# Kernel tuning notes

Hardware: AMD Instinct MI355X
Metric: run time of the kernel (lower is better)

## Reference

```python
import jax, jax.numpy as jnp
import numpy as np

B, S, DM = 2, 2048, 2048
H, KVH, HD = 16, 4, 128
REP = H // KVH  # kv_repeat_factor = 4
ROPE_BASE = 10000.0
EPS = 1e-6


def setup_inputs() -> dict:
    key = jax.random.key(0)
    k0, k1, k2, k3, k4 = jax.random.split(key, 5)
    w = lambda k, o, i: jax.random.normal(k, (o, i), jnp.float32) * (1.0 / np.sqrt(i))
    return {
        "x": jax.random.normal(k0, (B, S, DM), jnp.float32),
        "Wq": w(k1, H * HD, DM),
        "Wk": w(k2, KVH * HD, DM),
        "Wv": w(k3, KVH * HD, DM),
        "Wo": w(k4, DM, H * HD),
    }


def _rope_tables(seq_len, dim):
    inv_freq = 1.0 / (ROPE_BASE ** (jnp.arange(0, dim, 2, dtype=jnp.float32) / dim))
    t = jnp.arange(seq_len, dtype=jnp.float32)
    freqs = jnp.outer(t, inv_freq)            # [S, dim/2]
    emb = jnp.concatenate([freqs, freqs], -1)  # [S, dim]
    return jnp.cos(emb), jnp.sin(emb)


def _rotate_half(x):
    d = x.shape[-1] // 2
    return jnp.concatenate([-x[..., d:], x[..., :d]], axis=-1)


def reference(x, Wq, Wk, Wv, Wo):
    bsz, seq_len, _ = x.shape
    # projections (torch Linear: y = x @ W.T)
    q = (x @ Wq.T).reshape(bsz, seq_len, H, HD).transpose(0, 2, 1, 3)    # [B,H,S,D]
    k = (x @ Wk.T).reshape(bsz, seq_len, KVH, HD).transpose(0, 2, 1, 3)  # [B,KVH,S,D]
    v = (x @ Wv.T).reshape(bsz, seq_len, KVH, HD).transpose(0, 2, 1, 3)
    # rotary embeddings
    cos, sin = _rope_tables(seq_len, HD)  # [S,D]
    cos, sin = cos[None, None], sin[None, None]
    q = q * cos + _rotate_half(q) * sin
    k = k * cos + _rotate_half(k) * sin
    # GQA repeat (repeat_interleave on head dim)
    k = jnp.repeat(k, REP, axis=1)  # [B,H,S,D]
    v = jnp.repeat(v, REP, axis=1)
    # feature map
    qf = jax.nn.elu(q) + 1.0
    kf = jax.nn.elu(k) + 1.0
    # causal linear attention: recurrent kv-state scan over time
    qf_t = qf.transpose(2, 0, 1, 3)  # [S,B,H,D]
    kf_t = kf.transpose(2, 0, 1, 3)
    v_t = v.transpose(2, 0, 1, 3)

    def step(carry, inp):
        state, z = carry                       # [B,H,D,D], [B,H,D]
        q_s, k_s, v_s = inp                    # each [B,H,D]
        state = state + k_s[..., :, None] * v_s[..., None, :]
        z = z + k_s
        num = jnp.einsum('bhe,bhed->bhd', q_s, state)
        den = jnp.einsum('bhe,bhe->bh', q_s, z)[..., None] + EPS
        return (state, z), num / den

    init = (jnp.zeros((bsz, H, HD, HD), x.dtype), jnp.zeros((bsz, H, HD), x.dtype))
    _, out = jax.lax.scan(step, init, (qf_t, kf_t, v_t))  # [S,B,H,D]
    out = out.transpose(1, 0, 2, 3).reshape(bsz, seq_len, H * HD)
    return out @ Wo.T
```

## Files before the change

### kernel.cpp

```cpp
#include <hip/hip_runtime.h>
#include <math.h>
#include <stdint.h>

#define B_ 2
#define S_ 2048
#define H_ 16
#define KVH_ 4
#define HD_ 128
#define NC_ 16
#define CHK_ 128
#define EPS_ 1e-6f
#define GK_ 2048
#define NT_ (GK_ / 32)

typedef __attribute__((ext_vector_type(8))) short short8;
typedef __attribute__((ext_vector_type(4))) float f32x4;

#define GLOAD16(gsrc, sdst) \
    __builtin_amdgcn_global_load_lds((const __attribute__((address_space(1))) unsigned int*)(gsrc), \
                                     (__attribute__((address_space(3))) unsigned int*)(sdst), 16, 0, 0)

static __device__ __forceinline__ float bf2f(unsigned int u) {
    return __uint_as_float(u << 16);
}

static __device__ __forceinline__ void pack8(const float* v, uint4& hi, uint4& lo) {
    unsigned int h[4], l[4];
#pragma unroll
    for (int w = 0; w < 4; w++) {
        unsigned int b0 = __float_as_uint(v[2 * w]);
        unsigned int b1 = __float_as_uint(v[2 * w + 1]);
        unsigned int h0 = b0 & 0xFFFF0000u, h1 = b1 & 0xFFFF0000u;
        h[w] = (h0 >> 16) | h1;
        float r0 = v[2 * w] - __uint_as_float(h0);
        float r1 = v[2 * w + 1] - __uint_as_float(h1);
        l[w] = (__float_as_uint(r0) >> 16) | (__float_as_uint(r1) & 0xFFFF0000u);
    }
    hi = make_uint4(h[0], h[1], h[2], h[3]);
    lo = make_uint4(l[0], l[1], l[2], l[3]);
}

static __device__ __forceinline__ void split8_frag(const float* p, short8& hi, short8& lo) {
#pragma unroll
    for (int e = 0; e < 8; e++) {
        unsigned int b = __float_as_uint(p[e]);
        unsigned int h = b & 0xFFFF0000u;
        hi[e] = (short)(h >> 16);
        float r = p[e] - __uint_as_float(h);
        lo[e] = (short)(__float_as_uint(r) >> 16);
    }
}

__global__ __launch_bounds__(256) void rope_tables_k(float* __restrict__ cost,
                                                     float* __restrict__ sint) {
    int idx = blockIdx.x * 256 + threadIdx.x;
    int j = idx & 63;
    int s = idx >> 6;
    float inv_freq = powf(10000.0f, -(float)(2 * j) / 128.0f);
    float f = (float)s * inv_freq;
    cost[idx] = cosf(f);
    sint[idx] = sinf(f);
}

__global__ __launch_bounds__(256) void split_k(const float* __restrict__ in,
                                               unsigned int* __restrict__ outp, int ngrp)
{
    int g = blockIdx.x * 256 + threadIdx.x;
    if (g >= ngrp) return;
    const float* p = in + (size_t)g * 8;
    float x[8];
    *(float4*)&x[0] = *(const float4*)p;
    *(float4*)&x[4] = *(const float4*)(p + 4);
    uint4 hi, lo;
    pack8(x, hi, lo);
    unsigned int* op = outp + (size_t)g * 8;
    *(uint4*)op       = hi;
    *(uint4*)(op + 4) = lo;
}

__global__ __launch_bounds__(256, 2) void gemm3_k(
    const char* __restrict__ Apk, const char* __restrict__ W0,
    const char* __restrict__ W1, const char* __restrict__ W2,
    float* __restrict__ Y, int ldY, int nend0, int nend1, int nbx)
{
    __shared__ __attribute__((aligned(16))) char smem[65536];

    int nwg = gridDim.x;
    int bid = blockIdx.x;
    int swz = (bid & 7) * (nwg >> 3) + (bid >> 3);
    int by = swz / nbx, bx = swz % nbx;
    const int m0 = by * 128, n0 = bx * 128;

    const char* Wsel;
    int nw;
    if (n0 < nend0)      { Wsel = W0; nw = n0; }
    else if (n0 < nend1) { Wsel = W1; nw = n0 - nend0; }
    else                 { Wsel = W2; nw = n0 - nend1; }

    const int tid = threadIdx.x;
    const int lane = tid & 63;
    const int wv = tid >> 6;
    const int wr = wv >> 1, wc = wv & 1;

    const int r8 = lane >> 3, sl = lane & 7;
    const char* ap[4];
    const char* wp[4];
    int adst[4], wdst[4];
#pragma unroll
    for (int i = 0; i < 4; i++) {
        int rowA = wv * 32 + i * 8 + r8;
        ap[i] = Apk + (size_t)(m0 + rowA) * (GK_ * 4) + (size_t)((sl ^ (rowA & 7)) * 16);
        wp[i] = Wsel + (size_t)(nw + rowA) * (GK_ * 4) + (size_t)((sl ^ (rowA & 7)) * 16);
        adst[i] = wv * 4096 + i * 1024;
        wdst[i] = 16384 + wv * 4096 + i * 1024;
    }

    const int lrow = lane & 15, lg = lane >> 4, lc7 = lane & 7;
    const int aoff = (wr * 64 + lrow) * 128 + ((((lg << 1)) ^ lc7) << 4);
    const int woff = 16384 + (wc * 64 + lrow) * 128 + ((((lg << 1)) ^ lc7) << 4);

    f32x4 acc[4][4];
#pragma unroll
    for (int i = 0; i < 4; i++)
#pragma unroll
        for (int j = 0; j < 4; j++) acc[i][j] = (f32x4)(0.f);

#pragma unroll
    for (int i = 0; i < 4; i++) {
        GLOAD16(ap[i], smem + adst[i]);
        GLOAD16(wp[i], smem + wdst[i]);
    }
    __syncthreads();

    for (int kt = 0; kt < NT_; ++kt) {
        const int cur = kt & 1;
        if (kt + 1 < NT_) {
            const size_t koff = (size_t)(kt + 1) * 128;
            const int nb = (cur ^ 1) * 32768;
#pragma unroll
            for (int i = 0; i < 4; i++) {
                GLOAD16(ap[i] + koff, smem + nb + adst[i]);
                GLOAD16(wp[i] + koff, smem + nb + wdst[i]);
            }
        }
        const char* sb = smem + cur * 32768;
        short8 ah[4], al[4], bh[4], bl[4];
#pragma unroll
        for (int f = 0; f < 4; f++) {
            ah[f] = *(const short8*)(sb + (aoff)        + f * 2048);
            al[f] = *(const short8*)(sb + (aoff ^ 16)   + f * 2048);
            bh[f] = *(const short8*)(sb + (woff)        + f * 2048);
            bl[f] = *(const short8*)(sb + (woff ^ 16)   + f * 2048);
        }
#pragma unroll
        for (int i = 0; i < 4; i++)
#pragma unroll
            for (int j = 0; j < 4; j++) {
                acc[i][j] = __builtin_amdgcn_mfma_f32_16x16x32_bf16(ah[i], bh[j], acc[i][j], 0, 0, 0);
                acc[i][j] = __builtin_amdgcn_mfma_f32_16x16x32_bf16(ah[i], bl[j], acc[i][j], 0, 0, 0);
                acc[i][j] = __builtin_amdgcn_mfma_f32_16x16x32_bf16(al[i], bh[j], acc[i][j], 0, 0, 0);
            }
        __syncthreads();
    }

#pragma unroll
    for (int i = 0; i < 4; i++) {
        int r0 = m0 + wr * 64 + i * 16 + lg * 4;
#pragma unroll
        for (int j = 0; j < 4; j++) {
            int cc = n0 + wc * 64 + j * 16 + lrow;
            f32x4 v = acc[i][j];
            Y[(size_t)(r0 + 0) * ldY + cc] = v[0];
            Y[(size_t)(r0 + 1) * ldY + cc] = v[1];
            Y[(size_t)(r0 + 2) * ldY + cc] = v[2];
            Y[(size_t)(r0 + 3) * ldY + cc] = v[3];
        }
    }
}

__global__ __launch_bounds__(256) void rope_feat_k(
    const float* __restrict__ qkv, const float* __restrict__ cost,
    const float* __restrict__ sint, char* __restrict__ qfpk, char* __restrict__ kfpk)
{
    int idx = blockIdx.x * 256 + threadIdx.x;
    int g = idx & 15;
    int t = idx >> 4;
    int hh = t % 20;
    int t2 = t / 20;
    int s = t2 % S_;
    int b = t2 / S_;
    const float* row = qkv + (size_t)(b * S_ + s) * 3072;
    int col;
    char* outp;
    if (hh < H_) {
        col = hh * HD_;
        outp = qfpk + ((size_t)(b * H_ + hh) * S_ + s) * 512;
    } else {
        int kv = hh - H_;
        col = 2048 + kv * HD_;
        outp = kfpk + ((size_t)(b * KVH_ + kv) * S_ + s) * 512;
    }
    int d0 = g * 8;
    int dp = (g < 8) ? d0 + 64 : d0 - 64;
    int j0 = (g < 8) ? d0 : d0 - 64;
    float xa[8], xb[8], o[8];
    *(float4*)&xa[0] = *(const float4*)(row + col + d0);
    *(float4*)&xa[4] = *(const float4*)(row + col + d0 + 4);
    *(float4*)&xb[0] = *(const float4*)(row + col + dp);
    *(float4*)&xb[4] = *(const float4*)(row + col + dp + 4);
#pragma unroll
    for (int e = 0; e < 8; e++) {
        float cs = cost[s * 64 + j0 + e];
        float sn = sint[s * 64 + j0 + e];
        float v = (g < 8) ? (xa[e] * cs - xb[e] * sn) : (xa[e] * cs + xb[e] * sn);
        o[e] = v > 0.f ? v + 1.f : expf(v);
    }
    uint4 hi, lo;
    pack8(o, hi, lo);
    *(uint4*)(outp + g * 32)      = hi;
    *(uint4*)(outp + g * 32 + 16) = lo;
}

__global__ __launch_bounds__(256) void copy_v_k(const float* __restrict__ qkv,
                                                float* __restrict__ vv,
                                                char* __restrict__ vtpk)
{
    __shared__ __attribute__((aligned(16))) float Vt[CHK_][HD_ + 4];
    int bx = blockIdx.x;
    int st = bx & 15;
    int bkv = bx >> 4;
    int b = bkv >> 2, kv = bkv & 3;
    int tid = threadIdx.x;
#pragma unroll
    for (int it = 0; it < 16; it++) {
        int idx = it * 256 + tid;
        int r = idx >> 5, c4 = idx & 31;
        float4 v = *(const float4*)(qkv + (size_t)(b * S_ + st * CHK_ + r) * 3072 + 2560 + kv * HD_ + c4 * 4);
        *(float4*)(vv + ((size_t)bkv * S_ + st * CHK_ + r) * HD_ + c4 * 4) = v;
        *(float4*)&Vt[r][c4 * 4] = v;
    }
    __syncthreads();
#pragma unroll
    for (int it = 0; it < 2; it++) {
        int t2 = it * 256 + tid;
        int d = t2 & 127, sg = t2 >> 7;
#pragma unroll
        for (int kk = 0; kk < 4; kk++) {
            int kgl = sg * 4 + kk;
            float f[8];
#pragma unroll
            for (int e = 0; e < 8; e++) f[e] = Vt[kgl * 8 + e][d];
            uint4 hi, lo;
            pack8(f, hi, lo);
            char* op = vtpk + (size_t)bkv * 1048576 + (size_t)d * 8192 + (size_t)(st * 16 + kgl) * 32;
            *(uint4*)op        = hi;
            *(uint4*)(op + 16) = lo;
        }
    }
}

__global__ __launch_bounds__(256) void chunk_kv_k(
    const char* __restrict__ kfpk, const float* __restrict__ vv,
    float* __restrict__ kvc, float* __restrict__ zc)
{
    int bx = blockIdx.x;
    int c = bx % NC_;
    int bkv = bx / NC_;
    const char* kp = kfpk + ((size_t)bkv * S_ + c * CHK_) * 512;
    const float* vp = vv + ((size_t)bkv * S_ + c * CHK_) * HD_;
    __shared__ __attribute__((aligned(16))) float ks[CHK_][HD_ + 4];
    __shared__ __attribute__((aligned(16))) float vs[CHK_][HD_ + 4];
    int tid = threadIdx.x, tx = tid & 15, ty = tid >> 4;
#pragma unroll
    for (int it = 0; it < 8; it++) {
        int idx = it * 256 + tid;
        int r = idx >> 4, kg = idx & 15;
        const uint4* sp = (const uint4*)(kp + (size_t)r * 512 + kg * 32);
        uint4 hi = sp[0], lo = sp[1];
        float* d = &ks[r][kg * 8];
        d[0] = bf2f(hi.x & 0xFFFFu) + bf2f(lo.x & 0xFFFFu);
        d[1] = bf2f(hi.x >> 16)     + bf2f(lo.x >> 16);
        d[2] = bf2f(hi.y & 0xFFFFu) + bf2f(lo.y & 0xFFFFu);
        d[3] = bf2f(hi.y >> 16)     + bf2f(lo.y >> 16);
        d[4] = bf2f(hi.z & 0xFFFFu) + bf2f(lo.z & 0xFFFFu);
        d[5] = bf2f(hi.z >> 16)     + bf2f(lo.z >> 16);
        d[6] = bf2f(hi.w & 0xFFFFu) + bf2f(lo.w & 0xFFFFu);
        d[7] = bf2f(hi.w >> 16)     + bf2f(lo.w >> 16);
    }
#pragma unroll
    for (int it = 0; it < 16; it++) {
        int idx = it * 256 + tid;
        int r = idx >> 5, c4 = idx & 31;
        *(float4*)&vs[r][c4 * 4] = *(const float4*)(vp + (size_t)r * HD_ + c4 * 4);
    }
    __syncthreads();
    float acc[8][8];
#pragma unroll
    for (int i = 0; i < 8; i++)
#pragma unroll
        for (int j = 0; j < 8; j++) acc[i][j] = 0.f;
    for (int j = 0; j < CHK_; j++) {
        float a[8], b[8];
        *(float4*)&a[0] = *(const float4*)&ks[j][ty * 8];
        *(float4*)&a[4] = *(const float4*)&ks[j][ty * 8 + 4];
        *(float4*)&b[0] = *(const float4*)&vs[j][tx * 8];
        *(float4*)&b[4] = *(const float4*)&vs[j][tx * 8 + 4];
#pragma unroll
        for (int i = 0; i < 8; i++)
#pragma unroll
            for (int jj = 0; jj < 8; jj++)
                acc[i][jj] = fmaf(a[i], b[jj], acc[i][jj]);
    }
    float* outp = kvc + (size_t)bx * (HD_ * HD_);
#pragma unroll
    for (int i = 0; i < 8; i++) {
        float* op = outp + (size_t)(ty * 8 + i) * HD_ + tx * 8;
        *(float4*)op       = make_float4(acc[i][0], acc[i][1], acc[i][2], acc[i][3]);
        *(float4*)(op + 4) = make_float4(acc[i][4], acc[i][5], acc[i][6], acc[i][7]);
    }
    if (tid < CHK_) {
        float z = 0.f;
        for (int j = 0; j < CHK_; j++) z += ks[j][tid];
        zc[(size_t)bx * HD_ + tid] = z;
    }
}

__global__ __launch_bounds__(256) void chunk_scan_k(const float* __restrict__ kvc,
                                                    char* __restrict__ kvct,
                                                    float* __restrict__ zc)
{
    int bx = blockIdx.x;
    int bkv = bx >> 3, dg = bx & 7;
    int tid = threadIdx.x;
    int d = dg * 16 + (tid & 15);
    int g8 = tid >> 4;
    float acc[8];
#pragma unroll
    for (int i = 0; i < 8; i++) acc[i] = 0.f;
    float zacc = 0.f;
    for (int c = 0; c < NC_; c++) {
        size_t cb = (size_t)(bkv * NC_ + c);
        const float* p = kvc + cb * 16384;
        float cur[8];
#pragma unroll
        for (int i = 0; i < 8; i++) cur[i] = p[(g8 * 8 + i) * 128 + d];
        uint4 hi, lo;
        pack8(acc, hi, lo);
        char* op = kvct + cb * 65536 + (size_t)d * 512 + g8 * 32;
        *(uint4*)op        = hi;
        *(uint4*)(op + 16) = lo;
#pragma unroll
        for (int i = 0; i < 8; i++) acc[i] += cur[i];
        if (tid < 16) {
            float* zp = zc + cb * 128 + dg * 16 + tid;
            float zcur = *zp;
            *zp = zacc;
            zacc += zcur;
        }
    }
}

__global__ __launch_bounds__(256, 1) void chunk_out_k(
    const char* __restrict__ qfpk, const char* __restrict__ kfpk,
    const char* __restrict__ vtpk, const char* __restrict__ kvct,
    const float* __restrict__ zc, char* __restrict__ attnpk)
{
    __shared__ __attribute__((aligned(16))) char smem[100864];
    char*  stA  = smem;
    char*  stB  = smem + 16384;
    float* Pf   = (float*)(smem + 32768);
    float* zs   = (float*)(smem + 98304);
    float* rsum = (float*)(smem + 98816);
    float* den2 = (float*)(smem + 99840);
    float* den  = (float*)(smem + 100352);

    int bx = blockIdx.x;
    int c = bx & 15, h = (bx >> 4) & 15, b = bx >> 8;
    int kv = h >> 2;
    int bkv = b * KVH_ + kv;
    int bkvc = bkv * NC_ + c;
    const char* Qb  = qfpk + ((size_t)(b * H_ + h) * S_ + c * CHK_) * 512;
    const char* Kb  = kfpk + ((size_t)bkv * S_ + c * CHK_) * 512;
    const char* Vtb = vtpk + (size_t)bkv * 1048576 + (size_t)c * 512;
    const char* Spb = kvct + (size_t)bkvc * 65536;
    const float* zp = zc + (size_t)bkvc * 128;

    int tid = threadIdx.x;
    int lane = tid & 63, wv = tid >> 6;
    int wr = wv >> 1, wc = wv & 1;
    int lrow = lane & 15, lg = lane >> 4, l7 = lane & 7;

    if (tid < 32) *(float4*)(zs + tid * 4) = *(const float4*)(zp + tid * 4);

    const char *qsrc[4], *ksrc[4], *vsrc[4], *ssrc[4];
    char *adst[4], *bdst[4];
#pragma unroll
    for (int i = 0; i < 4; i++) {
        int row = wv * 32 + i * 8 + (lane >> 3);
        int sl = (lane & 7) ^ (row & 7);
        qsrc[i] = Qb  + (size_t)row * 512  + sl * 16;
        ksrc[i] = Kb  + (size_t)row * 512  + sl * 16;
        vsrc[i] = Vtb + (size_t)row * 8192 + sl * 16;
        ssrc[i] = Spb + (size_t)row * 512  + sl * 16;
        adst[i] = stA + wv * 4096 + i * 1024;
        bdst[i] = stB + wv * 4096 + i * 1024;
    }
    int aoffs[4], boffs[4];
#pragma unroll
    for (int f = 0; f < 4; f++) {
        aoffs[f] = (wr * 64 + f * 16 + lrow) * 128 + (((lg << 1) ^ l7) << 4);
        boffs[f] = (wc * 64 + f * 16 + lrow) * 128 + (((lg << 1) ^ l7) << 4);
    }

    f32x4 acc1[4][4];
#pragma unroll
    for (int i = 0; i < 4; i++)
#pragma unroll
        for (int j = 0; j < 4; j++) acc1[i][j] = (f32x4)(0.f);

    for (int s = 0; s < 4; s++) {
#pragma unroll
        for (int i = 0; i < 4; i++) {
            GLOAD16(qsrc[i] + s * 128, adst[i]);
            GLOAD16(ksrc[i] + s * 128, bdst[i]);
        }
        __syncthreads();
        short8 ah[4], al[4], bh[4], bl[4];
#pragma unroll
        for (int f = 0; f < 4; f++) {
            ah[f] = *(const short8*)(stA + aoffs[f]);
            al[f] = *(const short8*)(stA + (aoffs[f] ^ 16));
            bh[f] = *(const short8*)(stB + boffs[f]);
            bl[f] = *(const short8*)(stB + (boffs[f] ^ 16));
        }
#pragma unroll
        for (int i = 0; i < 4; i++)
#pragma unroll
            for (int j = 0; j < 4; j++) {
                acc1[i][j] = __builtin_amdgcn_mfma_f32_16x16x32_bf16(ah[i], bh[j], acc1[i][j], 0, 0, 0);
                acc1[i][j] = __builtin_amdgcn_mfma_f32_16x16x32_bf16(ah[i], bl[j], acc1[i][j], 0, 0, 0);
                acc1[i][j] = __builtin_amdgcn_mfma_f32_16x16x32_bf16(al[i], bh[j], acc1[i][j], 0, 0, 0);
            }
        __syncthreads();
    }

#pragma unroll
    for (int fi = 0; fi < 4; fi++) {
#pragma unroll
        for (int reg = 0; reg < 4; reg++) {
            int i = wr * 64 + fi * 16 + lg * 4 + reg;
            float rsv = 0.f;
#pragma unroll
            for (int fj = 0; fj < 4; fj++) {
                int j = wc * 64 + fj * 16 + lrow;
                float v = (j <= i) ? acc1[fi][fj][reg] : 0.f;
                rsv += v;
                Pf[i * 128 + (((j >> 3) ^ (i & 7)) << 3) + (j & 7)] = v;
            }
#pragma unroll
            for (int m = 1; m < 16; m <<= 1) rsv += __shfl_xor(rsv, m, 64);
            if (lrow == 0) rsum[i * 2 + wc] = rsv;
        }
    }

    f32x4 acc2[4][4];
#pragma unroll
    for (int i = 0; i < 4; i++)
#pragma unroll
        for (int j = 0; j < 4; j++) acc2[i][j] = (f32x4)(0.f);
    float d2a[4] = {0.f, 0.f, 0.f, 0.f};

    for (int s = 0; s < 4; s++) {
#pragma unroll
        for (int i = 0; i < 4; i++) {
            GLOAD16(qsrc[i] + s * 128, adst[i]);
            GLOAD16(ssrc[i] + s * 128, bdst[i]);
        }
        __syncthreads();
        short8 ah[4], al[4], bh[4], bl[4];
#pragma unroll
        for (int f = 0; f < 4; f++) {
            ah[f] = *(const short8*)(stA + aoffs[f]);
            al[f] = *(const short8*)(stA + (aoffs[f] ^ 16));
            bh[f] = *(const short8*)(stB + boffs[f]);
            bl[f] = *(const short8*)(stB + (boffs[f] ^ 16));
        }
        float zv[8];
#pragma unroll
        for (int e = 0; e < 8; e++) zv[e] = zs[s * 32 + lg * 8 + e];
#pragma unroll
        for (int f = 0; f < 4; f++)
#pragma unroll
            for (int e = 0; e < 8; e++)
                d2a[f] += (bf2f((unsigned int)(unsigned short)ah[f][e]) +
                           bf2f((unsigned int)(unsigned short)al[f][e])) * zv[e];
#pragma unroll
        for (int i = 0; i < 4; i++)
#pragma unroll
            for (int j = 0; j < 4; j++) {
                acc2[i][j] = __builtin_amdgcn_mfma_f32_16x16x32_bf16(ah[i], bh[j], acc2[i][j], 0, 0, 0);
                acc2[i][j] = __builtin_amdgcn_mfma_f32_16x16x32_bf16(ah[i], bl[j], acc2[i][j], 0, 0, 0);
                acc2[i][j] = __builtin_amdgcn_mfma_f32_16x16x32_bf16(al[i], bh[j], acc2[i][j], 0, 0, 0);
            }
        __syncthreads();
    }
#pragma unroll
    for (int f = 0; f < 4; f++) {
        float v = d2a[f];
        v += __shfl_xor(v, 16, 64);
        v += __shfl_xor(v, 32, 64);
        if (wc == 0 && lg == 0) den2[wr * 64 + f * 16 + lrow] = v;
    }

    for (int s = 0; s < 4; s++) {
#pragma unroll
        for (int i = 0; i < 4; i++) GLOAD16(vsrc[i] + s * 128, bdst[i]);
        __syncthreads();
        short8 ph[4], pl[4], bh[4], bl[4];
#pragma unroll
        for (int f = 0; f < 4; f++) {
            int i = wr * 64 + f * 16 + lrow;
            int g = (s * 4 + lg) ^ (i & 7);
            float pv[8];
            *(float4*)&pv[0] = *(const float4*)(Pf + i * 128 + g * 8);
            *(float4*)&pv[4] = *(const float4*)(Pf + i * 128 + g * 8 + 4);
            split8_frag(pv, ph[f], pl[f]);
            bh[f] = *(const short8*)(stB + boffs[f]);
            bl[f] = *(const short8*)(stB + (boffs[f] ^ 16));
        }
#pragma unroll
        for (int i = 0; i < 4; i++)
#pragma unroll
            for (int j = 0; j < 4; j++) {
                acc2[i][j] = __builtin_amdgcn_mfma_f32_16x16x32_bf16(ph[i], bh[j], acc2[i][j], 0, 0, 0);
                acc2[i][j] = __builtin_amdgcn_mfma_f32_16x16x32_bf16(ph[i], bl[j], acc2[i][j], 0, 0, 0);
                acc2[i][j] = __builtin_amdgcn_mfma_f32_16x16x32_bf16(pl[i], bh[j], acc2[i][j], 0, 0, 0);
            }
        __syncthreads();
    }

    if (tid < 128) den[tid] = rsum[tid * 2] + rsum[tid * 2 + 1] + den2[tid] + EPS_;
    __syncthreads();
#pragma unroll
    for (int fi = 0; fi < 4; fi++) {
#pragma unroll
        for (int reg = 0; reg < 4; reg++) {
            int i = wr * 64 + fi * 16 + lg * 4 + reg;
            float inv = 1.0f / den[i];
#pragma unroll
            for (int fd = 0; fd < 4; fd++) {
                int d = wc * 64 + fd * 16 + lrow;
                Pf[i * 128 + (((d >> 3) ^ (i & 7)) << 3) + (d & 7)] = acc2[fi][fd][reg] * inv;
            }
        }
    }
    __syncthreads();
    int s0 = c * CHK_;
#pragma unroll
    for (int it = 0; it < 8; it++) {
        int idx = it * 256 + tid;
        int row = idx >> 4, kg = idx & 15;
        int g = kg ^ (row & 7);
        float f[8];
        *(float4*)&f[0] = *(const float4*)(Pf + row * 128 + g * 8);
        *(float4*)&f[4] = *(const float4*)(Pf + row * 128 + g * 8 + 4);
        uint4 hi, lo;
        pack8(f, hi, lo);
        char* op = attnpk + ((size_t)(b * S_ + s0 + row) * 256 + h * 16 + kg) * 32;
        *(uint4*)op        = hi;
        *(uint4*)(op + 16) = lo;
    }
}

extern "C" void kernel_launch(void* const* d_in, const int* in_sizes, int n_in,
                              void* d_out, int out_size, void* d_ws, size_t ws_size,
                              hipStream_t stream)
{
    (void)in_sizes; (void)n_in; (void)out_size; (void)ws_size;
    const float* x  = (const float*)d_in[0];
    const float* Wq = (const float*)d_in[1];
    const float* Wk = (const float*)d_in[2];
    const float* Wv = (const float*)d_in[3];
    const float* Wo = (const float*)d_in[4];
    float* out = (float*)d_out;
    float* ws  = (float*)d_ws;

    float* xpk   = ws;
    float* wqpk  = ws + 8388608;
    float* wkpk  = ws + 12582912;
    float* wvpk  = ws + 13631488;
    float* qkv   = ws + 14680064;
    float* cost  = ws + 27262976;
    float* sint  = ws + 27394048;
    float* zc    = ws + 27525120;

    char*  qfpk   = (char*)xpk;
    char*  kfpk   = (char*)(ws + 8388608);
    float* vv     = ws + 10485760;
    char*  vtpk   = (char*)(ws + 12582912);
    float* kvc    = ws + 14680064;
    char*  kvct   = (char*)(ws + 16777216);
    char*  attnpk = (char*)(ws + 18874368);
    float* wopk   = ws + 14680064;

    rope_tables_k<<<512, 256, 0, stream>>>(cost, sint);

    split_k<<<4096, 256, 0, stream>>>(x,  (unsigned int*)xpk,  1048576);
    split_k<<<2048, 256, 0, stream>>>(Wq, (unsigned int*)wqpk, 524288);
    split_k<<<512,  256, 0, stream>>>(Wk, (unsigned int*)wkpk, 131072);
    split_k<<<512,  256, 0, stream>>>(Wv, (unsigned int*)wvpk, 131072);
    gemm3_k<<<768, 256, 0, stream>>>((const char*)xpk, (const char*)wqpk,
                                     (const char*)wkpk, (const char*)wvpk,
                                     qkv, 3072, 2048, 2560, 24);

    rope_feat_k<<<5120, 256, 0, stream>>>(qkv, cost, sint, qfpk, kfpk);
    copy_v_k<<<128, 256, 0, stream>>>(qkv, vv, vtpk);

    chunk_kv_k<<<B_ * KVH_ * NC_, 256, 0, stream>>>(kfpk, vv, kvc, zc);
    chunk_scan_k<<<64, 256, 0, stream>>>(kvc, kvct, zc);
    chunk_out_k<<<B_ * H_ * NC_, 256, 0, stream>>>(qfpk, kfpk, vtpk, kvct, zc, attnpk);

    split_k<<<2048, 256, 0, stream>>>(Wo, (unsigned int*)wopk, 524288);
    gemm3_k<<<512, 256, 0, stream>>>((const char*)attnpk, (const char*)wopk,
                                     (const char*)wopk, (const char*)wopk,
                                     out, 2048, 1 << 30, 1 << 30, 16);
}
```

Baseline: 459.1 us.

## Fuse RoPE/feature-map and V copy into QKV GEMM epilogue; merge input splits

The QKV GEMM epilogue now stages each output tile in shared memory and applies RoPE plus the elu+1 feature map directly, writing the packed bf16 hi/lo q/k buffers and the fp32 V layout. This removes the fp32 qkv intermediate and the separate rope_feat and V-copy passes. The four input split kernels are merged into one launch. Costs include a shared-memory round trip and an extra barrier in the GEMM epilogue, scattered cos/sin table reads there, and a rearranged workspace layout.

```diff
diff --git a/kernel.cpp b/kernel.cpp
--- a/kernel.cpp
+++ b/kernel.cpp
@@ -60,6 +60,31 @@
     float f = (float)s * inv_freq;
     cost[idx] = cosf(f);
     sint[idx] = sinf(f);
+}
+
+__global__ __launch_bounds__(256) void split_in_k(
+    const float* __restrict__ x,  const float* __restrict__ wq,
+    const float* __restrict__ wk, const float* __restrict__ wv,
+    unsigned int* __restrict__ xpk,  unsigned int* __restrict__ wqpk,
+    unsigned int* __restrict__ wkpk, unsigned int* __restrict__ wvpk)
+{
+    int g = blockIdx.x * 256 + threadIdx.x;
+    const float* in;
+    unsigned int* outp;
+    int lg;
+    if (g < 1048576)      { in = x;  outp = xpk;  lg = g; }
+    else if (g < 1572864) { in = wq; outp = wqpk; lg = g - 1048576; }
+    else if (g < 1703936) { in = wk; outp = wkpk; lg = g - 1572864; }
+    else                  { in = wv; outp = wvpk; lg = g - 1703936; }
+    const float* p = in + (size_t)lg * 8;
+    float v[8];
+    *(float4*)&v[0] = *(const float4*)p;
+    *(float4*)&v[4] = *(const float4*)(p + 4);
+    uint4 hi, lo;
+    pack8(v, hi, lo);
+    unsigned int* op = outp + (size_t)lg * 8;
+    *(uint4*)op       = hi;
+    *(uint4*)(op + 4) = lo;
 }
 
 __global__ __launch_bounds__(256) void split_k(const float* __restrict__ in,
@@ -78,10 +103,13 @@
     *(uint4*)(op + 4) = lo;
 }
 
+template <int EPI>
 __global__ __launch_bounds__(256, 2) void gemm3_k(
     const char* __restrict__ Apk, const char* __restrict__ W0,
     const char* __restrict__ W1, const char* __restrict__ W2,
-    float* __restrict__ Y, int ldY, int nend0, int nend1, int nbx)
+    float* __restrict__ Y, int ldY, int nend0, int nend1, int nbx,
+    const float* __restrict__ cosT, const float* __restrict__ sinT,
+    char* __restrict__ qfo, char* __restrict__ kfo, float* __restrict__ vvo)
 {
     __shared__ __attribute__((aligned(16))) char smem[65536];
 
@@ -163,81 +191,91 @@
         __syncthreads();
     }
 
-#pragma unroll
-    for (int i = 0; i < 4; i++) {
-        int r0 = m0 + wr * 64 + i * 16 + lg * 4;
-#pragma unroll
-        for (int j = 0; j < 4; j++) {
-            int cc = n0 + wc * 64 + j * 16 + lrow;
-            f32x4 v = acc[i][j];
-            Y[(size_t)(r0 + 0) * ldY + cc] = v[0];
-            Y[(size_t)(r0 + 1) * ldY + cc] = v[1];
-            Y[(size_t)(r0 + 2) * ldY + cc] = v[2];
-            Y[(size_t)(r0 + 3) * ldY + cc] = v[3];
-        }
-    }
-}
-
-__global__ __launch_bounds__(256) void rope_feat_k(
-    const float* __restrict__ qkv, const float* __restrict__ cost,
-    const float* __restrict__ sint, char* __restrict__ qfpk, char* __restrict__ kfpk)
-{
-    int idx = blockIdx.x * 256 + threadIdx.x;
-    int g = idx & 15;
-    int t = idx >> 4;
-    int hh = t % 20;
-    int t2 = t / 20;
-    int s = t2 % S_;
-    int b = t2 / S_;
-    const float* row = qkv + (size_t)(b * S_ + s) * 3072;
-    int col;
-    char* outp;
-    if (hh < H_) {
-        col = hh * HD_;
-        outp = qfpk + ((size_t)(b * H_ + hh) * S_ + s) * 512;
+    if (EPI == 0) {
+#pragma unroll
+        for (int i = 0; i < 4; i++) {
+            int r0 = m0 + wr * 64 + i * 16 + lg * 4;
+#pragma unroll
+            for (int j = 0; j < 4; j++) {
+                int cc = n0 + wc * 64 + j * 16 + lrow;
+                f32x4 v = acc[i][j];
+                Y[(size_t)(r0 + 0) * ldY + cc] = v[0];
+                Y[(size_t)(r0 + 1) * ldY + cc] = v[1];
+                Y[(size_t)(r0 + 2) * ldY + cc] = v[2];
+                Y[(size_t)(r0 + 3) * ldY + cc] = v[3];
+            }
+        }
     } else {
-        int kv = hh - H_;
-        col = 2048 + kv * HD_;
-        outp = kfpk + ((size_t)(b * KVH_ + kv) * S_ + s) * 512;
-    }
-    int d0 = g * 8;
-    int dp = (g < 8) ? d0 + 64 : d0 - 64;
-    int j0 = (g < 8) ? d0 : d0 - 64;
-    float xa[8], xb[8], o[8];
-    *(float4*)&xa[0] = *(const float4*)(row + col + d0);
-    *(float4*)&xa[4] = *(const float4*)(row + col + d0 + 4);
-    *(float4*)&xb[0] = *(const float4*)(row + col + dp);
-    *(float4*)&xb[4] = *(const float4*)(row + col + dp + 4);
-#pragma unroll
-    for (int e = 0; e < 8; e++) {
-        float cs = cost[s * 64 + j0 + e];
-        float sn = sint[s * 64 + j0 + e];
-        float v = (g < 8) ? (xa[e] * cs - xb[e] * sn) : (xa[e] * cs + xb[e] * sn);
-        o[e] = v > 0.f ? v + 1.f : expf(v);
-    }
-    uint4 hi, lo;
-    pack8(o, hi, lo);
-    *(uint4*)(outp + g * 32)      = hi;
-    *(uint4*)(outp + g * 32 + 16) = lo;
-}
-
-__global__ __launch_bounds__(256) void copy_v_k(const float* __restrict__ qkv,
-                                                float* __restrict__ vv,
-                                                char* __restrict__ vtpk)
+        float* Ct = (float*)smem;
+#pragma unroll
+        for (int i = 0; i < 4; i++) {
+            int r = wr * 64 + i * 16 + lg * 4;
+#pragma unroll
+            for (int j = 0; j < 4; j++) {
+                int ccol = wc * 64 + j * 16 + lrow;
+#pragma unroll
+                for (int rr = 0; rr < 4; rr++)
+                    Ct[(r + rr) * 128 + ccol] = acc[i][j][rr];
+            }
+        }
+        __syncthreads();
+        if (n0 < 2560) {
+            const int isq = (n0 < 2048) ? 1 : 0;
+            const int hh = isq ? (n0 >> 7) : ((n0 - 2048) >> 7);
+            char* basep = isq ? qfo : kfo;
+            const int bstride = (isq ? H_ : KVH_) * S_;
+#pragma unroll
+            for (int it = 0; it < 8; it++) {
+                int idx = it * 256 + tid;
+                int row = idx >> 4, g = idx & 15;
+                int midx = m0 + row, bb = midx >> 11, ss = midx & 2047;
+                int j0 = g * 8;
+                int lowh = (j0 < 64) ? 1 : 0;
+                int f0 = lowh ? j0 : j0 - 64;
+                float o[8];
+#pragma unroll
+                for (int e = 0; e < 8; e++) {
+                    float cs = cosT[ss * 64 + f0 + e];
+                    float sn = sinT[ss * 64 + f0 + e];
+                    float a = Ct[row * 128 + j0 + e];
+                    float p = Ct[row * 128 + (lowh ? j0 + e + 64 : j0 + e - 64)];
+                    float v = lowh ? (a * cs - p * sn) : (a * cs + p * sn);
+                    o[e] = v > 0.f ? v + 1.f : expf(v);
+                }
+                uint4 hi, lo;
+                pack8(o, hi, lo);
+                char* dst = basep + ((size_t)bb * bstride + (size_t)hh * S_ + ss) * 512 + g * 32;
+                *(uint4*)dst        = hi;
+                *(uint4*)(dst + 16) = lo;
+            }
+        } else {
+            const int kvh = (n0 - 2560) >> 7;
+#pragma unroll
+            for (int it = 0; it < 16; it++) {
+                int idx = it * 256 + tid;
+                int r = idx >> 5, c4 = idx & 31;
+                int midx = m0 + r, bb = midx >> 11, ss = midx & 2047;
+                *(float4*)(vvo + ((size_t)(bb * KVH_ + kvh) * S_ + ss) * HD_ + c4 * 4) =
+                    *(const float4*)(Ct + r * 128 + c4 * 4);
+            }
+        }
+    }
+}
+
+__global__ __launch_bounds__(256) void vt_k(const float* __restrict__ vv,
+                                            char* __restrict__ vtpk)
 {
     __shared__ __attribute__((aligned(16))) float Vt[CHK_][HD_ + 4];
     int bx = blockIdx.x;
     int st = bx & 15;
     int bkv = bx >> 4;
-    int b = bkv >> 2, kv = bkv & 3;
     int tid = threadIdx.x;
 #pragma unroll
     for (int it = 0; it < 16; it++) {
         int idx = it * 256 + tid;
         int r = idx >> 5, c4 = idx & 31;
-        float4 v = *(const float4*)(qkv + (size_t)(b * S_ + st * CHK_ + r) * 3072 + 2560 + kv * HD_ + c4 * 4);
-        *(float4*)(vv + ((size_t)bkv * S_ + st * CHK_ + r) * HD_ + c4 * 4) = v;
-        *(float4*)&Vt[r][c4 * 4] = v;
+        *(float4*)&Vt[r][c4 * 4] =
+            *(const float4*)(vv + ((size_t)bkv * S_ + st * CHK_ + r) * HD_ + c4 * 4);
     }
     __syncthreads();
 #pragma unroll
@@ -589,39 +627,37 @@
     float* wqpk  = ws + 8388608;
     float* wkpk  = ws + 12582912;
     float* wvpk  = ws + 13631488;
-    float* qkv   = ws + 14680064;
+    char*  qfpk  = (char*)(ws + 14680064);
+    char*  kfpk  = (char*)(ws + 23068672);
+    float* vv    = ws + 25165824;
     float* cost  = ws + 27262976;
     float* sint  = ws + 27394048;
     float* zc    = ws + 27525120;
-
-    char*  qfpk   = (char*)xpk;
-    char*  kfpk   = (char*)(ws + 8388608);
-    float* vv     = ws + 10485760;
-    char*  vtpk   = (char*)(ws + 12582912);
-    float* kvc    = ws + 14680064;
-    char*  kvct   = (char*)(ws + 16777216);
-    char*  attnpk = (char*)(ws + 18874368);
-    float* wopk   = ws + 14680064;
+    char*  vtpk   = (char*)(ws + 8388608);
+    float* kvc    = ws + 10485760;
+    char*  kvct   = (char*)(ws + 12582912);
+    char*  attnpk = (char*)ws;
+    float* wopk   = ws + 8388608;
 
     rope_tables_k<<<512, 256, 0, stream>>>(cost, sint);
 
-    split_k<<<4096, 256, 0, stream>>>(x,  (unsigned int*)xpk,  1048576);
-    split_k<<<2048, 256, 0, stream>>>(Wq, (unsigned int*)wqpk, 524288);
-    split_k<<<512,  256, 0, stream>>>(Wk, (unsigned int*)wkpk, 131072);
-    split_k<<<512,  256, 0, stream>>>(Wv, (unsigned int*)wvpk, 131072);
-    gemm3_k<<<768, 256, 0, stream>>>((const char*)xpk, (const char*)wqpk,
-                                     (const char*)wkpk, (const char*)wvpk,
-                                     qkv, 3072, 2048, 2560, 24);
-
-    rope_feat_k<<<5120, 256, 0, stream>>>(qkv, cost, sint, qfpk, kfpk);
-    copy_v_k<<<128, 256, 0, stream>>>(qkv, vv, vtpk);
+    split_in_k<<<7168, 256, 0, stream>>>(x, Wq, Wk, Wv,
+                                         (unsigned int*)xpk, (unsigned int*)wqpk,
+                                         (unsigned int*)wkpk, (unsigned int*)wvpk);
+    gemm3_k<1><<<768, 256, 0, stream>>>((const char*)xpk, (const char*)wqpk,
+                                        (const char*)wkpk, (const char*)wvpk,
+                                        nullptr, 0, 2048, 2560, 24,
+                                        cost, sint, qfpk, kfpk, vv);
+
+    vt_k<<<128, 256, 0, stream>>>(vv, vtpk);
 
     chunk_kv_k<<<B_ * KVH_ * NC_, 256, 0, stream>>>(kfpk, vv, kvc, zc);
     chunk_scan_k<<<64, 256, 0, stream>>>(kvc, kvct, zc);
     chunk_out_k<<<B_ * H_ * NC_, 256, 0, stream>>>(qfpk, kfpk, vtpk, kvct, zc, attnpk);
 
     split_k<<<2048, 256, 0, stream>>>(Wo, (unsigned int*)wopk, 524288);
-    gemm3_k<<<512, 256, 0, stream>>>((const char*)attnpk, (const char*)wopk,
-                                     (const char*)wopk, (const char*)wopk,
-                                     out, 2048, 1 << 30, 1 << 30, 16);
-}
+    gemm3_k<0><<<512, 256, 0, stream>>>((const char*)attnpk, (const char*)wopk,
+                                        (const char*)wopk, (const char*)wopk,
+                                        out, 2048, 1 << 30, 1 << 30, 16,
+                                        nullptr, nullptr, nullptr, nullptr, nullptr);
+}
```

Result: faster. 426.6 us (-7.1%).
